# Kernel optimization log

Measured on AMD Instinct MI355X. Metric: run time of the kernel, lower is better.

Reference implementation:

```python
import jax, jax.numpy as jnp
import numpy as np

N = 50000      # nodes per type
E = 600000     # edges per relation
D_IN = 128
D_OUT = 64


def setup_inputs() -> dict:
    key = jax.random.key(0)
    ks = jax.random.split(key, 12)
    x_v0 = jax.random.normal(ks[0], (N, D_IN), dtype=jnp.float32)
    x_v1 = jax.random.normal(ks[1], (N, D_IN), dtype=jnp.float32)
    edge_v0 = jax.random.randint(ks[2], (2, E), 0, N, dtype=jnp.int64)
    edge_v1 = jax.random.randint(ks[3], (2, E), 0, N, dtype=jnp.int64)
    s = 1.0 / np.sqrt(D_IN)
    Wrel0 = jax.random.uniform(ks[4], (D_OUT, D_IN), jnp.float32, -s, s)
    brel0 = jax.random.uniform(ks[5], (D_OUT,), jnp.float32, -s, s)
    Wroot0 = jax.random.uniform(ks[6], (D_OUT, D_IN), jnp.float32, -s, s)
    Wrel1 = jax.random.uniform(ks[7], (D_OUT, D_IN), jnp.float32, -s, s)
    brel1 = jax.random.uniform(ks[8], (D_OUT,), jnp.float32, -s, s)
    Wroot1 = jax.random.uniform(ks[9], (D_OUT, D_IN), jnp.float32, -s, s)
    sf = 1.0 / np.sqrt(2 * D_OUT)
    Wfc = jax.random.uniform(ks[10], (1, 2 * D_OUT), jnp.float32, -sf, sf)
    bfc = jax.random.uniform(ks[11], (1,), jnp.float32, -sf, sf)
    return {"x_v0": x_v0, "x_v1": x_v1, "edge_v0": edge_v0, "edge_v1": edge_v1,
            "Wrel0": Wrel0, "brel0": brel0, "Wroot0": Wroot0,
            "Wrel1": Wrel1, "brel1": brel1, "Wroot1": Wroot1,
            "Wfc": Wfc, "bfc": bfc}


def _graph_conv(x, edge_index, Wrel, brel, Wroot):
    # PyG GraphConv (aggr='add'): out = lin_rel(sum_{j in N(i)} x_j) + lin_root(x_i)
    src, dst = edge_index[0], edge_index[1]
    agg = jax.ops.segment_sum(x[src], dst, num_segments=x.shape[0])  # [N, D_IN]
    return agg @ Wrel.T + brel + x @ Wroot.T


def reference(x_v0, x_v1, edge_v0, edge_v1, Wrel0, brel0, Wroot0,
              Wrel1, brel1, Wroot1, Wfc, bfc):
    h0 = jax.nn.relu(_graph_conv(x_v0, edge_v0, Wrel0, brel0, Wroot0))  # [N, 64]
    h1 = jax.nn.relu(_graph_conv(x_v1, edge_v1, Wrel1, brel1, Wroot1))  # [N, 64]
    h = jnp.concatenate([h0, h1], axis=1)  # [N, 128]
    return h @ Wfc.T + bfc  # [N, 1]
```

## Files before the change

kernel.cpp:

```cpp
#include <hip/hip_runtime.h>
#include <hip/hip_bf16.h>

typedef __attribute__((ext_vector_type(8))) short short8;
typedef __attribute__((ext_vector_type(4))) short short4v;
typedef __attribute__((ext_vector_type(4))) float floatx4;

#define NB    1000
#define BPN   50
#define BCAP  832
#define PBLK  64
#define SCAP  32
#define BM    64

static __device__ __forceinline__ unsigned short bf16_of(float f) {
    union { float f; unsigned u; } v; v.f = f;
    unsigned r = (v.u + 0x7FFF + ((v.u >> 16) & 1)) >> 16;
    return (unsigned short)r;
}
static __device__ __forceinline__ float lo_f(unsigned u) {
    union { float f; unsigned u; } v; v.u = u << 16; return v.f;
}
static __device__ __forceinline__ float hi_f(unsigned u) {
    union { float f; unsigned u; } v; v.u = u & 0xFFFF0000u; return v.f;
}

__global__ __launch_bounds__(256) void convert_w(
    const float* __restrict__ Wrel0, const float* __restrict__ Wroot0,
    const float* __restrict__ Wrel1, const float* __restrict__ Wroot1,
    unsigned short* __restrict__ Wb0, unsigned short* __restrict__ Wb1)
{
    int c = blockIdx.x * 256 + threadIdx.x;
    if (c >= 4096) return;

    const float* s; unsigned short* d;
    if      (c < 1024) { s = Wrel0 + c * 8;           d = Wb0 + c * 8; }
    else if (c < 2048) { int t = c - 1024; s = Wroot0 + t * 8; d = Wb0 + 8192 + t * 8; }
    else if (c < 3072) { int t = c - 2048; s = Wrel1 + t * 8;  d = Wb1 + t * 8; }
    else               { int t = c - 3072; s = Wroot1 + t * 8; d = Wb1 + 8192 + t * 8; }

    floatx4 v0 = *(const floatx4*)s;
    floatx4 v1 = *(const floatx4*)(s + 4);
    short8 r = { (short)bf16_of(v0[0]), (short)bf16_of(v0[1]),
                 (short)bf16_of(v0[2]), (short)bf16_of(v0[3]),
                 (short)bf16_of(v1[0]), (short)bf16_of(v1[1]),
                 (short)bf16_of(v1[2]), (short)bf16_of(v1[3]) };
    *(short8*)d = r;
}

union SmemU {
    struct { short x_sh[BM * 136]; } g;
    struct { int lcur[NB]; } p;
};

__global__ __launch_bounds__(256) void gemm_and_pass(
    const float* __restrict__ X0, const float* __restrict__ X1,
    const unsigned short* __restrict__ Wb0, const unsigned short* __restrict__ Wb1,
    unsigned short* __restrict__ Yrel0, unsigned short* __restrict__ Yrel1,
    unsigned short* __restrict__ Yroot0, unsigned short* __restrict__ Yroot1,
    const int* __restrict__ e0, const int* __restrict__ e1,
    unsigned int* __restrict__ pairs0, unsigned int* __restrict__ pairs1,
    unsigned short* __restrict__ cnt0, unsigned short* __restrict__ cnt1,
    int E, int N)
{
    __shared__ __align__(16) SmemU sm;
    const int tid = threadIdx.x;
    const int rel = blockIdx.y;

    if (blockIdx.x < PBLK) {
        const int* e            = rel ? e1 : e0;
        unsigned int* pairs     = rel ? pairs1 : pairs0;
        unsigned short* cnt     = rel ? cnt1 : cnt0;
        const int blk           = blockIdx.x;

        const int epb = (E + PBLK - 1) / PBLK;
        const int s0  = blk * epb;
        const int s1  = min(s0 + epb, E);

        for (int b = tid; b < NB; b += 256) sm.p.lcur[b] = 0;
        __syncthreads();

        for (int i = s0 + tid; i < s1; i += 256) {
            int dst = e[E + i];
            if ((unsigned)dst < (unsigned)N) {
                int src = e[i];
                unsigned usrc = ((unsigned)src < (unsigned)N) ? (unsigned)src : 0u;
                int b = (unsigned)dst / BPN;
                int pos = atomicAdd(&sm.p.lcur[b], 1);
                if (pos < SCAP)
                    pairs[(((size_t)blk * NB + b) << 5) + pos] =
                        ((unsigned)dst << 16) | usrc;
            }
        }
        __syncthreads();

        for (int b = tid; b < NB; b += 256)
            cnt[b * PBLK + blk] = (unsigned short)min(sm.p.lcur[b], SCAP);
        return;
    }

    const float* X           = rel ? X1 : X0;
    const unsigned short* Wb = rel ? Wb1 : Wb0;
    unsigned short* Yrel     = rel ? Yrel1 : Yrel0;
    unsigned short* Yroot    = rel ? Yroot1 : Yroot0;

    const int m0   = (blockIdx.x - PBLK) * BM;
    const int w    = tid >> 6;
    const int lane = tid & 63;
    const int q    = lane >> 4;
    const int r    = lane & 15;

    short8 bw[2][4];
#pragma unroll
    for (int nt = 0; nt < 2; ++nt)
#pragma unroll
        for (int ko = 0; ko < 4; ++ko)
            bw[nt][ko] = *(const short8*)(Wb + (w * 32 + nt * 16 + r) * 128 + ko * 32 + q * 8);

#pragma unroll
    for (int i = 0; i < 8; ++i) {
        int c    = tid + 256 * i;
        int row  = c >> 5;
        int f    = (c & 31) * 4;
        int node = m0 + row;
        floatx4 v = {};
        if (node < N) v = *(const floatx4*)(X + (size_t)node * 128 + f);
        short4v sv = { (short)bf16_of(v[0]), (short)bf16_of(v[1]),
                       (short)bf16_of(v[2]), (short)bf16_of(v[3]) };
        *(short4v*)&sm.g.x_sh[row * 136 + f] = sv;
    }
    __syncthreads();

    floatx4 acc[4][2] = {};
#pragma unroll
    for (int ko = 0; ko < 4; ++ko) {
        int kb = ko * 32 + q * 8;
        short8 a[4];
#pragma unroll
        for (int mt = 0; mt < 4; ++mt)
            a[mt] = *(const short8*)&sm.g.x_sh[(mt * 16 + r) * 136 + kb];
#pragma unroll
        for (int mt = 0; mt < 4; ++mt) {
            acc[mt][0] = __builtin_amdgcn_mfma_f32_16x16x32_bf16(a[mt], bw[0][ko], acc[mt][0], 0, 0, 0);
            acc[mt][1] = __builtin_amdgcn_mfma_f32_16x16x32_bf16(a[mt], bw[1][ko], acc[mt][1], 0, 0, 0);
        }
    }

    unsigned short* Yp = (w < 2) ? Yrel : Yroot;
    const int cbase = (w & 1) * 32;
#pragma unroll
    for (int mt = 0; mt < 4; ++mt)
#pragma unroll
        for (int nt = 0; nt < 2; ++nt) {
            int col = cbase + nt * 16 + r;
#pragma unroll
            for (int reg = 0; reg < 4; ++reg) {
                int node = m0 + mt * 16 + q * 4 + reg;
                if (node < N) Yp[(size_t)node * 64 + col] = bf16_of(acc[mt][nt][reg]);
            }
        }
}

__global__ __launch_bounds__(512) void bucket_gather(
    const unsigned int* __restrict__ pairs0, const unsigned int* __restrict__ pairs1,
    const unsigned short* __restrict__ cnt0, const unsigned short* __restrict__ cnt1,
    const unsigned short* __restrict__ Yrel0, const unsigned short* __restrict__ Yrel1,
    const unsigned short* __restrict__ Yroot0, const unsigned short* __restrict__ Yroot1,
    const float* __restrict__ brel0, const float* __restrict__ brel1,
    const float* __restrict__ wfc, const float* __restrict__ bfc,
    float* __restrict__ out, int N)
{
    __shared__ unsigned short slist0[BCAP], slist1[BCAP];
    __shared__ unsigned short scnt0[PBLK], scnt1[PBLK];
    __shared__ int cnt0s[BPN], cnt1s[BPN];
    __shared__ int off0s[BPN], off1s[BPN];
    __shared__ int cur0s[BPN], cur1s[BPN];

    const int tid  = threadIdx.x;
    const int b    = blockIdx.x;
    const int wv   = tid >> 6;
    const int lane = tid & 63;
    const int c    = lane & 31;
    const int half = lane >> 5;

    if (tid < PBLK)            scnt0[tid] = cnt0[b * PBLK + tid];
    else if (tid < 2 * PBLK)   scnt1[tid - PBLK] = cnt1[b * PBLK + (tid - PBLK)];
    for (int i = tid; i < BPN; i += 512) { cnt0s[i] = 0; cnt1s[i] = 0; }
    __syncthreads();

    const unsigned base = (unsigned)(b * BPN);

    for (int j = tid; j < PBLK * SCAP; j += 512) {
        int blk = j >> 5, k = j & 31;
        if (k < (int)scnt0[blk]) {
            unsigned p = pairs0[(((size_t)blk * NB + b) << 5) + k];
            atomicAdd(&cnt0s[(p >> 16) - base], 1);
        }
    }
    for (int j = tid; j < PBLK * SCAP; j += 512) {
        int blk = j >> 5, k = j & 31;
        if (k < (int)scnt1[blk]) {
            unsigned p = pairs1[(((size_t)blk * NB + b) << 5) + k];
            atomicAdd(&cnt1s[(p >> 16) - base], 1);
        }
    }
    __syncthreads();

    if (wv == 0) {
        int cc = (lane < BPN) ? cnt0s[lane] : 0;
        int inc = cc;
#pragma unroll
        for (int d = 1; d < 64; d <<= 1) {
            int t = __shfl_up(inc, d, 64);
            if (lane >= d) inc += t;
        }
        if (lane < BPN) { off0s[lane] = inc - cc; cur0s[lane] = inc - cc; }
    } else if (wv == 1) {
        int cc = (lane < BPN) ? cnt1s[lane] : 0;
        int inc = cc;
#pragma unroll
        for (int d = 1; d < 64; d <<= 1) {
            int t = __shfl_up(inc, d, 64);
            if (lane >= d) inc += t;
        }
        if (lane < BPN) { off1s[lane] = inc - cc; cur1s[lane] = inc - cc; }
    }
    __syncthreads();

    for (int j = tid; j < PBLK * SCAP; j += 512) {
        int blk = j >> 5, k = j & 31;
        if (k < (int)scnt0[blk]) {
            unsigned p = pairs0[(((size_t)blk * NB + b) << 5) + k];
            int pos = atomicAdd(&cur0s[(p >> 16) - base], 1);
            if (pos < BCAP) slist0[pos] = (unsigned short)(p & 0xFFFFu);
        }
    }
    for (int j = tid; j < PBLK * SCAP; j += 512) {
        int blk = j >> 5, k = j & 31;
        if (k < (int)scnt1[blk]) {
            unsigned p = pairs1[(((size_t)blk * NB + b) << 5) + k];
            int pos = atomicAdd(&cur1s[(p >> 16) - base], 1);
            if (pos < BCAP) slist1[pos] = (unsigned short)(p & 0xFFFFu);
        }
    }
    __syncthreads();

    const float2 br0 = ((const float2*)brel0)[c];
    const float2 br1 = ((const float2*)brel1)[c];
    const float2 w0  = ((const float2*)wfc)[c];
    const float2 w1  = ((const float2*)(wfc + 64))[c];
    const float bias = bfc[0];

    for (int nl = wv; nl < BPN; nl += 8) {
        int i = b * BPN + nl;
        float a0x = 0.f, a0y = 0.f, a1x = 0.f, a1y = 0.f;

        {
            int st = off0s[nl], d = cnt0s[nl], j = 0;
            for (; j + 7 < d; j += 8) {
                int i0 = slist0[st + j + half];
                int i1 = slist0[st + j + 2 + half];
                int i2 = slist0[st + j + 4 + half];
                int i3 = slist0[st + j + 6 + half];
                unsigned u0 = ((const unsigned*)(Yrel0 + ((size_t)i0 << 6)))[c];
                unsigned u1 = ((const unsigned*)(Yrel0 + ((size_t)i1 << 6)))[c];
                unsigned u2 = ((const unsigned*)(Yrel0 + ((size_t)i2 << 6)))[c];
                unsigned u3 = ((const unsigned*)(Yrel0 + ((size_t)i3 << 6)))[c];
                a0x += (lo_f(u0) + lo_f(u1)) + (lo_f(u2) + lo_f(u3));
                a0y += (hi_f(u0) + hi_f(u1)) + (hi_f(u2) + hi_f(u3));
            }
            for (; j < d; j += 2) {
                int jj = j + half;
                int idx = slist0[st + (jj < d ? jj : d - 1)];
                unsigned u = ((const unsigned*)(Yrel0 + ((size_t)idx << 6)))[c];
                if (jj < d) { a0x += lo_f(u); a0y += hi_f(u); }
            }
        }
        {
            int st = off1s[nl], d = cnt1s[nl], j = 0;
            for (; j + 7 < d; j += 8) {
                int i0 = slist1[st + j + half];
                int i1 = slist1[st + j + 2 + half];
                int i2 = slist1[st + j + 4 + half];
                int i3 = slist1[st + j + 6 + half];
                unsigned u0 = ((const unsigned*)(Yrel1 + ((size_t)i0 << 6)))[c];
                unsigned u1 = ((const unsigned*)(Yrel1 + ((size_t)i1 << 6)))[c];
                unsigned u2 = ((const unsigned*)(Yrel1 + ((size_t)i2 << 6)))[c];
                unsigned u3 = ((const unsigned*)(Yrel1 + ((size_t)i3 << 6)))[c];
                a1x += (lo_f(u0) + lo_f(u1)) + (lo_f(u2) + lo_f(u3));
                a1y += (hi_f(u0) + hi_f(u1)) + (hi_f(u2) + hi_f(u3));
            }
            for (; j < d; j += 2) {
                int jj = j + half;
                int idx = slist1[st + (jj < d ? jj : d - 1)];
                unsigned u = ((const unsigned*)(Yrel1 + ((size_t)idx << 6)))[c];
                if (jj < d) { a1x += lo_f(u); a1y += hi_f(u); }
            }
        }

        a0x += __shfl_xor(a0x, 32, 64);
        a0y += __shfl_xor(a0y, 32, 64);
        a1x += __shfl_xor(a1x, 32, 64);
        a1y += __shfl_xor(a1y, 32, 64);

        unsigned ur0 = ((const unsigned*)(Yroot0 + ((size_t)i << 6)))[c];
        unsigned ur1 = ((const unsigned*)(Yroot1 + ((size_t)i << 6)))[c];

        float h0x = fmaxf(a0x + br0.x + lo_f(ur0), 0.f);
        float h0y = fmaxf(a0y + br0.y + hi_f(ur0), 0.f);
        float h1x = fmaxf(a1x + br1.x + lo_f(ur1), 0.f);
        float h1y = fmaxf(a1y + br1.y + hi_f(ur1), 0.f);
        float s = h0x * w0.x + h0y * w0.y + h1x * w1.x + h1y * w1.y;

#pragma unroll
        for (int m = 16; m > 0; m >>= 1) s += __shfl_xor(s, m, 64);
        if (lane == 0) out[i] = s + bias;
    }
}

extern "C" void kernel_launch(void* const* d_in, const int* in_sizes, int n_in,
                              void* d_out, int out_size, void* d_ws, size_t ws_size,
                              hipStream_t stream)
{
    const int N = in_sizes[0] / 128;
    const int E = in_sizes[2] / 2;

    const float* x0     = (const float*)d_in[0];
    const float* x1     = (const float*)d_in[1];
    const int*   e0     = (const int*)d_in[2];
    const int*   e1     = (const int*)d_in[3];
    const float* Wrel0  = (const float*)d_in[4];
    const float* brel0  = (const float*)d_in[5];
    const float* Wroot0 = (const float*)d_in[6];
    const float* Wrel1  = (const float*)d_in[7];
    const float* brel1  = (const float*)d_in[8];
    const float* Wroot1 = (const float*)d_in[9];
    const float* wfc    = (const float*)d_in[10];
    const float* bfc    = (const float*)d_in[11];
    float* out = (float*)d_out;

    unsigned short* Wb0    = (unsigned short*)d_ws;
    unsigned short* Wb1    = Wb0 + 128 * 128;
    unsigned short* Yrel0  = Wb1 + 128 * 128;
    unsigned short* Yrel1  = Yrel0 + (size_t)N * 64;
    unsigned short* Yroot0 = Yrel1 + (size_t)N * 64;
    unsigned short* Yroot1 = Yroot0 + (size_t)N * 64;
    unsigned int* pairs0   = (unsigned int*)(Yroot1 + (size_t)N * 64);
    unsigned int* pairs1   = pairs0 + (size_t)PBLK * NB * SCAP;
    unsigned short* cnt0   = (unsigned short*)(pairs1 + (size_t)PBLK * NB * SCAP);
    unsigned short* cnt1   = cnt0 + (size_t)NB * PBLK;

    convert_w<<<16, 256, 0, stream>>>(Wrel0, Wroot0, Wrel1, Wroot1, Wb0, Wb1);

    const int gemm_nblk = (N + BM - 1) / BM;
    dim3 fused_grid(PBLK + gemm_nblk, 2);
    gemm_and_pass<<<fused_grid, 256, 0, stream>>>(
        x0, x1, Wb0, Wb1, Yrel0, Yrel1, Yroot0, Yroot1,
        e0, e1, pairs0, pairs1, cnt0, cnt1, E, N);

    bucket_gather<<<NB, 512, 0, stream>>>(pairs0, pairs1, cnt0, cnt1,
                                          Yrel0, Yrel1, Yroot0, Yroot1,
                                          brel0, brel1, wfc, bfc, out, N);
}
```

Before: 200.0 us.

## Spread edge partitioning over more blocks and compact bucket reads via prefix sums

Raises the number of partition blocks per relation from 64 to 160 and lowers the per-slot capacity from 32 to 24. The partition loop is unrolled four ways so each thread issues several edge loads before its shared-memory atomics. In the gather kernel, each bucket block builds a prefix sum over the per-partition counts and binary-searches it. Threads then walk only the valid pairs instead of every (partition, slot) position. This is meant to raise parallelism in the partition phase and cut idle iterations in the gather phase, at the cost of an 8-step search per pair. The smaller per-slot capacity raises the risk of silently dropping edges when a bucket's slot overflows.

After: 182.2 us. -8.9%, faster.

```diff
diff --git a/kernel.cpp b/kernel.cpp
--- a/kernel.cpp
+++ b/kernel.cpp
@@ -8,8 +8,8 @@
 #define NB    1000
 #define BPN   50
 #define BCAP  832
-#define PBLK  64
-#define SCAP  32
+#define PBLK  160
+#define SCAP  24
 #define BM    64
 
 static __device__ __forceinline__ unsigned short bf16_of(float f) {
@@ -67,10 +67,10 @@
     const int rel = blockIdx.y;
 
     if (blockIdx.x < PBLK) {
-        const int* e            = rel ? e1 : e0;
-        unsigned int* pairs     = rel ? pairs1 : pairs0;
-        unsigned short* cnt     = rel ? cnt1 : cnt0;
-        const int blk           = blockIdx.x;
+        const int* e        = rel ? e1 : e0;
+        unsigned int* pairs = rel ? pairs1 : pairs0;
+        unsigned short* cnt = rel ? cnt1 : cnt0;
+        const int blk       = blockIdx.x;
 
         const int epb = (E + PBLK - 1) / PBLK;
         const int s0  = blk * epb;
@@ -79,17 +79,28 @@
         for (int b = tid; b < NB; b += 256) sm.p.lcur[b] = 0;
         __syncthreads();
 
-        for (int i = s0 + tid; i < s1; i += 256) {
-            int dst = e[E + i];
-            if ((unsigned)dst < (unsigned)N) {
-                int src = e[i];
-                unsigned usrc = ((unsigned)src < (unsigned)N) ? (unsigned)src : 0u;
-                int b = (unsigned)dst / BPN;
-                int pos = atomicAdd(&sm.p.lcur[b], 1);
-                if (pos < SCAP)
-                    pairs[(((size_t)blk * NB + b) << 5) + pos] =
-                        ((unsigned)dst << 16) | usrc;
-            }
+        for (int i = s0 + tid; i < s1; i += 256 * 4) {
+            const int i1 = i + 256, i2 = i + 512, i3 = i + 768;
+            int d0 = e[E + i];
+            int sA = e[i];
+            int d1 = (i1 < s1) ? e[E + i1] : -1;
+            int sB = (i1 < s1) ? e[i1] : 0;
+            int d2 = (i2 < s1) ? e[E + i2] : -1;
+            int sC = (i2 < s1) ? e[i2] : 0;
+            int d3 = (i3 < s1) ? e[E + i3] : -1;
+            int sD = (i3 < s1) ? e[i3] : 0;
+
+#define PROC(dd, ss)                                                         \
+            if ((unsigned)(dd) < (unsigned)N) {                              \
+                unsigned usrc = ((unsigned)(ss) < (unsigned)N) ? (unsigned)(ss) : 0u; \
+                int b_ = (unsigned)(dd) / BPN;                               \
+                int pos = atomicAdd(&sm.p.lcur[b_], 1);                      \
+                if (pos < SCAP)                                              \
+                    pairs[((size_t)blk * NB + b_) * SCAP + pos] =            \
+                        ((unsigned)(dd) << 16) | usrc;                       \
+            }
+            PROC(d0, sA) PROC(d1, sB) PROC(d2, sC) PROC(d3, sD)
+#undef PROC
         }
         __syncthreads();
 
@@ -170,7 +181,7 @@
     float* __restrict__ out, int N)
 {
     __shared__ unsigned short slist0[BCAP], slist1[BCAP];
-    __shared__ unsigned short scnt0[PBLK], scnt1[PBLK];
+    __shared__ int pref0[PBLK + 1], pref1[PBLK + 1];
     __shared__ int cnt0s[BPN], cnt1s[BPN];
     __shared__ int off0s[BPN], off1s[BPN];
     __shared__ int cur0s[BPN], cur1s[BPN];
@@ -182,26 +193,76 @@
     const int c    = lane & 31;
     const int half = lane >> 5;
 
-    if (tid < PBLK)            scnt0[tid] = cnt0[b * PBLK + tid];
-    else if (tid < 2 * PBLK)   scnt1[tid - PBLK] = cnt1[b * PBLK + (tid - PBLK)];
     for (int i = tid; i < BPN; i += 512) { cnt0s[i] = 0; cnt1s[i] = 0; }
+
+    if (wv == 0) {
+        int cv[3], ssum = 0;
+#pragma unroll
+        for (int t = 0; t < 3; ++t) {
+            int idx = lane * 3 + t;
+            cv[t] = (idx < PBLK) ? (int)cnt0[b * PBLK + idx] : 0;
+            ssum += cv[t];
+        }
+        int inc = ssum;
+#pragma unroll
+        for (int d = 1; d < 64; d <<= 1) {
+            int t = __shfl_up(inc, d, 64);
+            if (lane >= d) inc += t;
+        }
+        int ex = inc - ssum;
+#pragma unroll
+        for (int t = 0; t < 3; ++t) {
+            int idx = lane * 3 + t;
+            if (idx <= PBLK) pref0[idx] = ex;
+            ex += cv[t];
+        }
+    } else if (wv == 1) {
+        int cv[3], ssum = 0;
+#pragma unroll
+        for (int t = 0; t < 3; ++t) {
+            int idx = lane * 3 + t;
+            cv[t] = (idx < PBLK) ? (int)cnt1[b * PBLK + idx] : 0;
+            ssum += cv[t];
+        }
+        int inc = ssum;
+#pragma unroll
+        for (int d = 1; d < 64; d <<= 1) {
+            int t = __shfl_up(inc, d, 64);
+            if (lane >= d) inc += t;
+        }
+        int ex = inc - ssum;
+#pragma unroll
+        for (int t = 0; t < 3; ++t) {
+            int idx = lane * 3 + t;
+            if (idx <= PBLK) pref1[idx] = ex;
+            ex += cv[t];
+        }
+    }
     __syncthreads();
 
     const unsigned base = (unsigned)(b * BPN);
-
-    for (int j = tid; j < PBLK * SCAP; j += 512) {
-        int blk = j >> 5, k = j & 31;
-        if (k < (int)scnt0[blk]) {
-            unsigned p = pairs0[(((size_t)blk * NB + b) << 5) + k];
-            atomicAdd(&cnt0s[(p >> 16) - base], 1);
-        }
-    }
-    for (int j = tid; j < PBLK * SCAP; j += 512) {
-        int blk = j >> 5, k = j & 31;
-        if (k < (int)scnt1[blk]) {
-            unsigned p = pairs1[(((size_t)blk * NB + b) << 5) + k];
-            atomicAdd(&cnt1s[(p >> 16) - base], 1);
-        }
+    const int tot0 = pref0[PBLK];
+    const int tot1 = pref1[PBLK];
+
+    for (int j = tid; j < tot0; j += 512) {
+        int lo = 0, hi = PBLK;
+#pragma unroll
+        for (int it = 0; it < 8; ++it) {
+            int mid = (lo + hi) >> 1;
+            if (pref0[mid] <= j) lo = mid; else hi = mid;
+        }
+        unsigned p = pairs0[((size_t)lo * NB + b) * SCAP + (j - pref0[lo])];
+        atomicAdd(&cnt0s[(p >> 16) - base], 1);
+    }
+    for (int j = tid; j < tot1; j += 512) {
+        int lo = 0, hi = PBLK;
+#pragma unroll
+        for (int it = 0; it < 8; ++it) {
+            int mid = (lo + hi) >> 1;
+            if (pref1[mid] <= j) lo = mid; else hi = mid;
+        }
+        unsigned p = pairs1[((size_t)lo * NB + b) * SCAP + (j - pref1[lo])];
+        atomicAdd(&cnt1s[(p >> 16) - base], 1);
     }
     __syncthreads();
 
@@ -226,21 +287,27 @@
     }
     __syncthreads();
 
-    for (int j = tid; j < PBLK * SCAP; j += 512) {
-        int blk = j >> 5, k = j & 31;
-        if (k < (int)scnt0[blk]) {
-            unsigned p = pairs0[(((size_t)blk * NB + b) << 5) + k];
-            int pos = atomicAdd(&cur0s[(p >> 16) - base], 1);
-            if (pos < BCAP) slist0[pos] = (unsigned short)(p & 0xFFFFu);
-        }
-    }
-    for (int j = tid; j < PBLK * SCAP; j += 512) {
-        int blk = j >> 5, k = j & 31;
-        if (k < (int)scnt1[blk]) {
-            unsigned p = pairs1[(((size_t)blk * NB + b) << 5) + k];
-            int pos = atomicAdd(&cur1s[(p >> 16) - base], 1);
-            if (pos < BCAP) slist1[pos] = (unsigned short)(p & 0xFFFFu);
-        }
+    for (int j = tid; j < tot0; j += 512) {
+        int lo = 0, hi = PBLK;
+#pragma unroll
+        for (int it = 0; it < 8; ++it) {
+            int mid = (lo + hi) >> 1;
+            if (pref0[mid] <= j) lo = mid; else hi = mid;
+        }
+        unsigned p = pairs0[((size_t)lo * NB + b) * SCAP + (j - pref0[lo])];
+        int pos = atomicAdd(&cur0s[(p >> 16) - base], 1);
+        if (pos < BCAP) slist0[pos] = (unsigned short)(p & 0xFFFFu);
+    }
+    for (int j = tid; j < tot1; j += 512) {
+        int lo = 0, hi = PBLK;
+#pragma unroll
+        for (int it = 0; it < 8; ++it) {
+            int mid = (lo + hi) >> 1;
+            if (pref1[mid] <= j) lo = mid; else hi = mid;
+        }
+        unsigned p = pairs1[((size_t)lo * NB + b) * SCAP + (j - pref1[lo])];
+        int pos = atomicAdd(&cur1s[(p >> 16) - base], 1);
+        if (pos < BCAP) slist1[pos] = (unsigned short)(p & 0xFFFFu);
     }
     __syncthreads();
 
```

## Replace per-bucket CSR build with direct LDS atomic accumulation in gather

Applied to the files above, without the earlier changes.

The gather kernel no longer counts, prefix-sums and scatters the pairs into a per-node source list in shared memory. Each wave now walks the pair lists from its partition sub-blocks and atomically adds the gathered bf16 Yrel rows into per-node float accumulators in LDS, prefetching one row ahead. The count array layout is transposed to [blk][bucket] and the partition loop is unrolled by four to issue more edge loads at once. This removes several synchronised passes and the per-bucket capacity limit, at the cost of one LDS float atomic per edge per lane and serial per-wave row loads.

Measured after the change: 563.9 us. 182% more time.

```diff
diff --git a/kernel.cpp b/kernel.cpp
--- a/kernel.cpp
+++ b/kernel.cpp
@@ -7,7 +7,6 @@
 
 #define NB    1000
 #define BPN   50
-#define BCAP  832
 #define PBLK  64
 #define SCAP  32
 #define BM    64
@@ -19,9 +18,6 @@
 }
 static __device__ __forceinline__ float lo_f(unsigned u) {
     union { float f; unsigned u; } v; v.u = u << 16; return v.f;
-}
-static __device__ __forceinline__ float hi_f(unsigned u) {
-    union { float f; unsigned u; } v; v.u = u & 0xFFFF0000u; return v.f;
 }
 
 __global__ __launch_bounds__(256) void convert_w(
@@ -67,10 +63,10 @@
     const int rel = blockIdx.y;
 
     if (blockIdx.x < PBLK) {
-        const int* e            = rel ? e1 : e0;
-        unsigned int* pairs     = rel ? pairs1 : pairs0;
-        unsigned short* cnt     = rel ? cnt1 : cnt0;
-        const int blk           = blockIdx.x;
+        const int* e        = rel ? e1 : e0;
+        unsigned int* pairs = rel ? pairs1 : pairs0;
+        unsigned short* cnt = rel ? cnt1 : cnt0;
+        const int blk       = blockIdx.x;
 
         const int epb = (E + PBLK - 1) / PBLK;
         const int s0  = blk * epb;
@@ -79,22 +75,33 @@
         for (int b = tid; b < NB; b += 256) sm.p.lcur[b] = 0;
         __syncthreads();
 
-        for (int i = s0 + tid; i < s1; i += 256) {
-            int dst = e[E + i];
-            if ((unsigned)dst < (unsigned)N) {
-                int src = e[i];
-                unsigned usrc = ((unsigned)src < (unsigned)N) ? (unsigned)src : 0u;
-                int b = (unsigned)dst / BPN;
-                int pos = atomicAdd(&sm.p.lcur[b], 1);
-                if (pos < SCAP)
-                    pairs[(((size_t)blk * NB + b) << 5) + pos] =
-                        ((unsigned)dst << 16) | usrc;
-            }
+        for (int i = s0 + tid; i < s1; i += 256 * 4) {
+            const int i1 = i + 256, i2 = i + 512, i3 = i + 768;
+            int d0 = e[E + i];
+            int sA = e[i];
+            int d1 = (i1 < s1) ? e[E + i1] : -1;
+            int sB = (i1 < s1) ? e[i1] : 0;
+            int d2 = (i2 < s1) ? e[E + i2] : -1;
+            int sC = (i2 < s1) ? e[i2] : 0;
+            int d3 = (i3 < s1) ? e[E + i3] : -1;
+            int sD = (i3 < s1) ? e[i3] : 0;
+
+#define PROC(dd, ss)                                                         \
+            if ((unsigned)(dd) < (unsigned)N) {                              \
+                unsigned usrc = ((unsigned)(ss) < (unsigned)N) ? (unsigned)(ss) : 0u; \
+                int b_ = (unsigned)(dd) / BPN;                               \
+                int pos = atomicAdd(&sm.p.lcur[b_], 1);                      \
+                if (pos < SCAP)                                              \
+                    pairs[((size_t)blk * NB + b_) * SCAP + pos] =            \
+                        ((unsigned)(dd) << 16) | usrc;                       \
+            }
+            PROC(d0, sA) PROC(d1, sB) PROC(d2, sC) PROC(d3, sD)
+#undef PROC
         }
         __syncthreads();
 
         for (int b = tid; b < NB; b += 256)
-            cnt[b * PBLK + blk] = (unsigned short)min(sm.p.lcur[b], SCAP);
+            cnt[blk * NB + b] = (unsigned short)min(sm.p.lcur[b], SCAP);
         return;
     }
 
@@ -169,150 +176,77 @@
     const float* __restrict__ wfc, const float* __restrict__ bfc,
     float* __restrict__ out, int N)
 {
-    __shared__ unsigned short slist0[BCAP], slist1[BCAP];
-    __shared__ unsigned short scnt0[PBLK], scnt1[PBLK];
-    __shared__ int cnt0s[BPN], cnt1s[BPN];
-    __shared__ int off0s[BPN], off1s[BPN];
-    __shared__ int cur0s[BPN], cur1s[BPN];
+    __shared__ float acc0[BPN][64];
+    __shared__ float acc1[BPN][64];
 
     const int tid  = threadIdx.x;
     const int b    = blockIdx.x;
     const int wv   = tid >> 6;
     const int lane = tid & 63;
-    const int c    = lane & 31;
-    const int half = lane >> 5;
-
-    if (tid < PBLK)            scnt0[tid] = cnt0[b * PBLK + tid];
-    else if (tid < 2 * PBLK)   scnt1[tid - PBLK] = cnt1[b * PBLK + (tid - PBLK)];
-    for (int i = tid; i < BPN; i += 512) { cnt0s[i] = 0; cnt1s[i] = 0; }
+
+    for (int i = tid; i < BPN * 64; i += 512) {
+        ((float*)acc0)[i] = 0.f;
+        ((float*)acc1)[i] = 0.f;
+    }
     __syncthreads();
 
     const unsigned base = (unsigned)(b * BPN);
 
-    for (int j = tid; j < PBLK * SCAP; j += 512) {
-        int blk = j >> 5, k = j & 31;
-        if (k < (int)scnt0[blk]) {
-            unsigned p = pairs0[(((size_t)blk * NB + b) << 5) + k];
-            atomicAdd(&cnt0s[(p >> 16) - base], 1);
-        }
-    }
-    for (int j = tid; j < PBLK * SCAP; j += 512) {
-        int blk = j >> 5, k = j & 31;
-        if (k < (int)scnt1[blk]) {
-            unsigned p = pairs1[(((size_t)blk * NB + b) << 5) + k];
-            atomicAdd(&cnt1s[(p >> 16) - base], 1);
+#pragma unroll 1
+    for (int t = 0; t < 8; ++t) {
+        const int s  = wv + t * 8;
+        const int cs = (int)cnt0[s * NB + b];
+        const unsigned* ps = pairs0 + ((size_t)s * NB + b) * SCAP;
+        if (cs > 0) {
+            unsigned p0 = ps[0];
+            float y0 = lo_f((unsigned)Yrel0[(((size_t)(p0 & 0xFFFFu)) << 6) + lane]);
+            for (int k = 0; k < cs; ++k) {
+                unsigned p1 = 0; float y1 = 0.f;
+                if (k + 1 < cs) {
+                    p1 = ps[k + 1];
+                    y1 = lo_f((unsigned)Yrel0[(((size_t)(p1 & 0xFFFFu)) << 6) + lane]);
+                }
+                atomicAdd(&acc0[(p0 >> 16) - base][lane], y0);
+                p0 = p1; y0 = y1;
+            }
+        }
+    }
+#pragma unroll 1
+    for (int t = 0; t < 8; ++t) {
+        const int s  = wv + t * 8;
+        const int cs = (int)cnt1[s * NB + b];
+        const unsigned* ps = pairs1 + ((size_t)s * NB + b) * SCAP;
+        if (cs > 0) {
+            unsigned p0 = ps[0];
+            float y0 = lo_f((unsigned)Yrel1[(((size_t)(p0 & 0xFFFFu)) << 6) + lane]);
+            for (int k = 0; k < cs; ++k) {
+                unsigned p1 = 0; float y1 = 0.f;
+                if (k + 1 < cs) {
+                    p1 = ps[k + 1];
+                    y1 = lo_f((unsigned)Yrel1[(((size_t)(p1 & 0xFFFFu)) << 6) + lane]);
+                }
+                atomicAdd(&acc1[(p0 >> 16) - base][lane], y0);
+                p0 = p1; y0 = y1;
+            }
         }
     }
     __syncthreads();
 
-    if (wv == 0) {
-        int cc = (lane < BPN) ? cnt0s[lane] : 0;
-        int inc = cc;
-#pragma unroll
-        for (int d = 1; d < 64; d <<= 1) {
-            int t = __shfl_up(inc, d, 64);
-            if (lane >= d) inc += t;
-        }
-        if (lane < BPN) { off0s[lane] = inc - cc; cur0s[lane] = inc - cc; }
-    } else if (wv == 1) {
-        int cc = (lane < BPN) ? cnt1s[lane] : 0;
-        int inc = cc;
-#pragma unroll
-        for (int d = 1; d < 64; d <<= 1) {
-            int t = __shfl_up(inc, d, 64);
-            if (lane >= d) inc += t;
-        }
-        if (lane < BPN) { off1s[lane] = inc - cc; cur1s[lane] = inc - cc; }
-    }
-    __syncthreads();
-
-    for (int j = tid; j < PBLK * SCAP; j += 512) {
-        int blk = j >> 5, k = j & 31;
-        if (k < (int)scnt0[blk]) {
-            unsigned p = pairs0[(((size_t)blk * NB + b) << 5) + k];
-            int pos = atomicAdd(&cur0s[(p >> 16) - base], 1);
-            if (pos < BCAP) slist0[pos] = (unsigned short)(p & 0xFFFFu);
-        }
-    }
-    for (int j = tid; j < PBLK * SCAP; j += 512) {
-        int blk = j >> 5, k = j & 31;
-        if (k < (int)scnt1[blk]) {
-            unsigned p = pairs1[(((size_t)blk * NB + b) << 5) + k];
-            int pos = atomicAdd(&cur1s[(p >> 16) - base], 1);
-            if (pos < BCAP) slist1[pos] = (unsigned short)(p & 0xFFFFu);
-        }
-    }
-    __syncthreads();
-
-    const float2 br0 = ((const float2*)brel0)[c];
-    const float2 br1 = ((const float2*)brel1)[c];
-    const float2 w0  = ((const float2*)wfc)[c];
-    const float2 w1  = ((const float2*)(wfc + 64))[c];
+    const float br0 = brel0[lane];
+    const float br1 = brel1[lane];
+    const float w0  = wfc[lane];
+    const float w1  = wfc[64 + lane];
     const float bias = bfc[0];
 
     for (int nl = wv; nl < BPN; nl += 8) {
         int i = b * BPN + nl;
-        float a0x = 0.f, a0y = 0.f, a1x = 0.f, a1y = 0.f;
-
-        {
-            int st = off0s[nl], d = cnt0s[nl], j = 0;
-            for (; j + 7 < d; j += 8) {
-                int i0 = slist0[st + j + half];
-                int i1 = slist0[st + j + 2 + half];
-                int i2 = slist0[st + j + 4 + half];
-                int i3 = slist0[st + j + 6 + half];
-                unsigned u0 = ((const unsigned*)(Yrel0 + ((size_t)i0 << 6)))[c];
-                unsigned u1 = ((const unsigned*)(Yrel0 + ((size_t)i1 << 6)))[c];
-                unsigned u2 = ((const unsigned*)(Yrel0 + ((size_t)i2 << 6)))[c];
-                unsigned u3 = ((const unsigned*)(Yrel0 + ((size_t)i3 << 6)))[c];
-                a0x += (lo_f(u0) + lo_f(u1)) + (lo_f(u2) + lo_f(u3));
-                a0y += (hi_f(u0) + hi_f(u1)) + (hi_f(u2) + hi_f(u3));
-            }
-            for (; j < d; j += 2) {
-                int jj = j + half;
-                int idx = slist0[st + (jj < d ? jj : d - 1)];
-                unsigned u = ((const unsigned*)(Yrel0 + ((size_t)idx << 6)))[c];
-                if (jj < d) { a0x += lo_f(u); a0y += hi_f(u); }
-            }
-        }
-        {
-            int st = off1s[nl], d = cnt1s[nl], j = 0;
-            for (; j + 7 < d; j += 8) {
-                int i0 = slist1[st + j + half];
-                int i1 = slist1[st + j + 2 + half];
-                int i2 = slist1[st + j + 4 + half];
-                int i3 = slist1[st + j + 6 + half];
-                unsigned u0 = ((const unsigned*)(Yrel1 + ((size_t)i0 << 6)))[c];
-                unsigned u1 = ((const unsigned*)(Yrel1 + ((size_t)i1 << 6)))[c];
-                unsigned u2 = ((const unsigned*)(Yrel1 + ((size_t)i2 << 6)))[c];
-                unsigned u3 = ((const unsigned*)(Yrel1 + ((size_t)i3 << 6)))[c];
-                a1x += (lo_f(u0) + lo_f(u1)) + (lo_f(u2) + lo_f(u3));
-                a1y += (hi_f(u0) + hi_f(u1)) + (hi_f(u2) + hi_f(u3));
-            }
-            for (; j < d; j += 2) {
-                int jj = j + half;
-                int idx = slist1[st + (jj < d ? jj : d - 1)];
-                unsigned u = ((const unsigned*)(Yrel1 + ((size_t)idx << 6)))[c];
-                if (jj < d) { a1x += lo_f(u); a1y += hi_f(u); }
-            }
-        }
-
-        a0x += __shfl_xor(a0x, 32, 64);
-        a0y += __shfl_xor(a0y, 32, 64);
-        a1x += __shfl_xor(a1x, 32, 64);
-        a1y += __shfl_xor(a1y, 32, 64);
-
-        unsigned ur0 = ((const unsigned*)(Yroot0 + ((size_t)i << 6)))[c];
-        unsigned ur1 = ((const unsigned*)(Yroot1 + ((size_t)i << 6)))[c];
-
-        float h0x = fmaxf(a0x + br0.x + lo_f(ur0), 0.f);
-        float h0y = fmaxf(a0y + br0.y + hi_f(ur0), 0.f);
-        float h1x = fmaxf(a1x + br1.x + lo_f(ur1), 0.f);
-        float h1y = fmaxf(a1y + br1.y + hi_f(ur1), 0.f);
-        float s = h0x * w0.x + h0y * w0.y + h1x * w1.x + h1y * w1.y;
-
-#pragma unroll
-        for (int m = 16; m > 0; m >>= 1) s += __shfl_xor(s, m, 64);
+        float r0 = lo_f((unsigned)Yroot0[(size_t)i * 64 + lane]);
+        float r1 = lo_f((unsigned)Yroot1[(size_t)i * 64 + lane]);
+        float h0 = fmaxf(acc0[nl][lane] + br0 + r0, 0.f);
+        float h1 = fmaxf(acc1[nl][lane] + br1 + r1, 0.f);
+        float s = h0 * w0 + h1 * w1;
+#pragma unroll
+        for (int m = 32; m > 0; m >>= 1) s += __shfl_xor(s, m, 64);
         if (lane == 0) out[i] = s + bias;
     }
 }
```
